# Kernel tuning notes

Measured on AMD Instinct MI355X. Metric: run time of the kernel, lower is better.

The kernel has to match this reference:

```python
import jax, jax.numpy as jnp
import numpy as np
from jax import lax

B, D, L = 32, 256, 4096
Q, H, T = D // 4, D // 2, 3 * D // 4


def setup_inputs() -> dict:
    key = jax.random.key(0)
    ks = iter(jax.random.split(key, 64))

    def nrm(shape, s=0.02):
        return jax.random.normal(next(ks), shape, jnp.float32) * s

    inp = {"x": jax.random.normal(next(ks), (B, D, L), jnp.float32)}

    def pw(name, o, c):  # pointwise conv: weight [O,C], bias [O]
        inp[name + "_w"] = nrm((o, c))
        inp[name + "_b"] = jnp.zeros((o,), jnp.float32)

    def dw(name, c, k):  # depthwise conv: weight [C,1,K], bias [C]
        inp[name + "_w"] = nrm((c, 1, k))
        inp[name + "_b"] = jnp.zeros((c,), jnp.float32)

    inp["ln1_w"] = jnp.ones((D,), jnp.float32); inp["ln1_b"] = jnp.zeros((D,), jnp.float32)
    pw("a1p", Q, Q); dw("a1d", Q, 7)
    pw("v1", Q, Q); pw("v11", Q, Q); pw("v12", Q, Q)
    dw("c31", Q, 3)
    inp["ln2_w"] = jnp.ones((H,), jnp.float32); inp["ln2_b"] = jnp.zeros((H,), jnp.float32)
    pw("a2p", H, H); dw("a2d", H, 9)
    pw("v2", H, H); pw("v21", H, H); pw("v22", Q, Q)
    pw("p2", Q, H)
    dw("c32", Q, 3)
    inp["ln3_w"] = jnp.ones((T,), jnp.float32); inp["ln3_b"] = jnp.zeros((T,), jnp.float32)
    pw("a3p", T, T); dw("a3d", T, 11)
    pw("v3", T, T); pw("v31", T, T); pw("v32", Q, Q)
    pw("p3", Q, T)
    dw("c33", Q, 3)
    return inp


def _ln_cf(x, w, b, eps=1e-6):
    # channels_first LayerNorm: normalize over channel dim (axis=1)
    u = jnp.mean(x, axis=1, keepdims=True)
    s = jnp.mean((x - u) ** 2, axis=1, keepdims=True)
    return w[:, None] * (x - u) / jnp.sqrt(s + eps) + b[:, None]


def _pw(x, w, b):
    # 1x1 conv1d: x [B,C,L], w [O,C] -> [B,O,L]
    return jnp.einsum('bcl,oc->bol', x, w) + b[:, None]


def _dw(x, w, b, pad):
    # depthwise conv1d: x [B,C,L], w [C,1,K]
    y = lax.conv_general_dilated(x, w, (1,), [(pad, pad)],
                                 dimension_numbers=('NCH', 'OIH', 'NCH'),
                                 feature_group_count=x.shape[1])
    return y + b[:, None]


def reference(x, ln1_w, ln1_b, a1p_w, a1p_b, a1d_w, a1d_b, v1_w, v1_b,
              v11_w, v11_b, v12_w, v12_b, c31_w, c31_b,
              ln2_w, ln2_b, a2p_w, a2p_b, a2d_w, a2d_b, v2_w, v2_b,
              v21_w, v21_b, v22_w, v22_b, p2_w, p2_b, c32_w, c32_b,
              ln3_w, ln3_b, a3p_w, a3p_b, a3d_w, a3d_b, v3_w, v3_b,
              v31_w, v31_b, v32_w, v32_b, p3_w, p3_b, c33_w, c33_b):
    x = _ln_cf(x, ln1_w, ln1_b)
    xs = jnp.split(x, 4, axis=1)  # 4 chunks of Q channels

    # stage 1
    a = _dw(jax.nn.gelu(_pw(xs[0], a1p_w, a1p_b), approximate=False), a1d_w, a1d_b, 3)
    mul = _pw(a * _pw(xs[0], v1_w, v1_b), v11_w, v11_b)
    x1 = _dw(_pw(xs[1], v12_w, v12_b), c31_w, c31_b, 1) + a
    x1 = jnp.concatenate([x1, mul], axis=1)  # [B,H,L]

    # stage 2
    x1 = _ln_cf(x1, ln2_w, ln2_b)
    a = _dw(jax.nn.gelu(_pw(x1, a2p_w, a2p_b), approximate=False), a2d_w, a2d_b, 4)
    mul = _pw(a * _pw(x1, v2_w, v2_b), v21_w, v21_b)
    x2 = _dw(_pw(xs[2], v22_w, v22_b), c32_w, c32_b, 1) + _pw(a, p2_w, p2_b)
    x2 = jnp.concatenate([x2, mul], axis=1)  # [B,T,L]

    # stage 3
    x2 = _ln_cf(x2, ln3_w, ln3_b)
    a = _dw(jax.nn.gelu(_pw(x2, a3p_w, a3p_b), approximate=False), a3d_w, a3d_b, 5)
    mul = _pw(a * _pw(x2, v3_w, v3_b), v31_w, v31_b)
    x3 = _dw(_pw(xs[3], v32_w, v32_b), c33_w, c33_b, 1) + _pw(a, p3_w, p3_b)
    return jnp.concatenate([x3, mul], axis=1)  # [B,D,L]
```

## Files before the change

kernel.cpp:

```cpp
#include <hip/hip_runtime.h>
#include <cmath>


using u16 = unsigned short;
typedef short shrt8 __attribute__((ext_vector_type(8)));
typedef short shrt4 __attribute__((ext_vector_type(4)));
typedef float f32x4 __attribute__((ext_vector_type(4)));

#define DEVI __device__ __forceinline__

static constexpr int TL   = 64;
static constexpr int EXT  = 88;
static constexpr int RS   = 72;
static constexpr int SLOT = EXT * RS;
static constexpr int NW   = 8;
static constexpr int NTHR = 512;

DEVI u16 f2bf(float f) {
    unsigned u = __float_as_uint(f);
    u += 0x7FFFu + ((u >> 16) & 1u);
    return (u16)(u >> 16);
}
DEVI float bf2f(u16 h) { return __uint_as_float(((unsigned)h) << 16); }

DEVI float gelu_f(float x) {
    const float y  = x * 0.70710678118654752f;
    const float ay = fabsf(y);
    const float t  = __builtin_amdgcn_rcpf(fmaf(0.3275911f, ay, 1.0f));
    float p = 1.061405429f;
    p = fmaf(p, t, -1.453152027f);
    p = fmaf(p, t,  1.421413741f);
    p = fmaf(p, t, -0.284496736f);
    p = fmaf(p, t,  0.254829592f);
    float er = 1.0f - p * t * __expf(-ay * ay);
    er = copysignf(er, y);
    return 0.5f * x * (1.0f + er);
}

struct SL { int a, b, c; };
DEVI int slotOf(SL s, int ch) { return ch < 64 ? s.a : (ch < 128 ? s.b : s.c); }

template<int O, int C, int OSPLIT, bool GELU, bool TOG, bool INPL, bool LNF>
DEVI void pw_mfma(u16* sh, SL in, SL outA, SL outB, const u16* Wb,
                  const float* biasA, const float* biasB,
                  int elo, int ehi, int l0,
                  const float* uv = nullptr, const float* rsA = nullptr,
                  const float* mrsA = nullptr,
                  float* outg = nullptr, int bidx = 0, int ochan = 0) {
    constexpr int MR = O / 64;
    constexpr int KT = C / 32;
    constexpr int NT = 3;
    const int lane = threadIdx.x & 63;
    const int wv   = threadIdx.x >> 6;
    const int mw = wv >> 1, nw = wv & 1;
    const int col  = lane & 15;
    const int quad = lane >> 4;
    const int mrow = mw * (MR * 16) + col;
    const int kq   = quad * 8;
    const int crow = mw * (MR * 16) + quad * 4;

    f32x4 acc[MR][NT];
    #pragma unroll
    for (int mi = 0; mi < MR; ++mi) {
        f32x4 bv;
        if (LNF) { bv[0] = 0.f; bv[1] = 0.f; bv[2] = 0.f; bv[3] = 0.f; }
        else {
            const int ch = crow + mi * 16;
            const float* bp = (OSPLIT < O && ch >= OSPLIT) ? (biasB + (ch - OSPLIT))
                                                           : (biasA + ch);
            bv = *(const f32x4*)bp;
        }
        #pragma unroll
        for (int ni = 0; ni < NT; ++ni) acc[mi][ni] = bv;
    }
    bool act[NT]; int bpos[NT];
    #pragma unroll
    for (int ni = 0; ni < NT; ++ni) {
        const int nt = nw * NT + ni;
        act[ni] = (nt * 16 < ehi) && (nt * 16 + 16 > elo);
        int p = nt * 16 + col; if (p > EXT - 1) p = EXT - 1;
        bpos[ni] = p;
    }
    __builtin_amdgcn_s_setprio(1);
    #pragma unroll
    for (int kt = 0; kt < KT; ++kt) {
        shrt8 af[MR];
        #pragma unroll
        for (int mi = 0; mi < MR; ++mi)
            af[mi] = *(const shrt8*)(Wb + (size_t)(mrow + mi * 16) * C + kt * 32 + kq);
        const int k0 = kt * 32;
        const u16* bs = sh + slotOf(in, k0) * SLOT + ((k0 & 63) + kq);
        #pragma unroll
        for (int ni = 0; ni < NT; ++ni) {
            if (!act[ni]) continue;
            const shrt8 bf = *(const shrt8*)(bs + bpos[ni] * RS);
            #pragma unroll
            for (int mi = 0; mi < MR; ++mi)
                acc[mi][ni] = __builtin_amdgcn_mfma_f32_16x16x32_bf16(af[mi], bf, acc[mi][ni], 0, 0, 0);
        }
    }
    __builtin_amdgcn_s_setprio(0);
    if (INPL) __syncthreads();
    float rsv[NT], mrsv[NT];
    if (LNF) {
        #pragma unroll
        for (int ni = 0; ni < NT; ++ni) {
            rsv[ni]  = rsA[bpos[ni]];
            mrsv[ni] = mrsA[bpos[ni]];
        }
    }
    #pragma unroll
    for (int mi = 0; mi < MR; ++mi) {
        const int ch = crow + mi * 16;
        const bool isA = !(OSPLIT < O) || (ch < OSPLIT);
        f32x4 u4, v4;
        if (LNF) {
            u4 = *(const f32x4*)(uv + ch);
            v4 = *(const f32x4*)(uv + O + ch);
        }
        #pragma unroll
        for (int ni = 0; ni < NT; ++ni) {
            if (!act[ni]) continue;
            const int e = (nw * NT + ni) * 16 + col;
            if (e < elo || e >= ehi) continue;
            const int l = l0 + e;
            f32x4 v = acc[mi][ni];
            if (LNF) {
                #pragma unroll
                for (int i = 0; i < 4; ++i)
                    v[i] = fmaf(rsv[ni], v[i], fmaf(-mrsv[ni], v4[i], u4[i]));
            }
            if (GELU && isA) { v[0]=gelu_f(v[0]); v[1]=gelu_f(v[1]); v[2]=gelu_f(v[2]); v[3]=gelu_f(v[3]); }
            if (TOG) {
                float* og = outg + ((size_t)bidx * 256 + ochan + ch) * 4096 + l;
                og[0] = v[0]; og[4096] = v[1]; og[2*4096] = v[2]; og[3*4096] = v[3];
            } else {
                const int cl = isA ? ch : ch - OSPLIT;
                const SL  os = isA ? outA : outB;
                const bool gv = (unsigned)l < 4096u;
                shrt4 pk;
                pk[0] = gv ? (short)f2bf(v[0]) : (short)0;
                pk[1] = gv ? (short)f2bf(v[1]) : (short)0;
                pk[2] = gv ? (short)f2bf(v[2]) : (short)0;
                pk[3] = gv ? (short)f2bf(v[3]) : (short)0;
                *(shrt4*)(sh + slotOf(os, cl) * SLOT + e * RS + (cl & 63)) = pk;
            }
        }
    }
}

template<int C, int K, int PAD, int WIN, bool INPL>
DEVI void dw_mul(u16* sh, SL g, SL ao, SL v, const float* W, const float* bias,
                 int elo, int ehi) {
    const int lane = threadIdx.x & 63;
    const int wv   = threadIdx.x >> 6;
    const int nwin  = (ehi - elo + WIN - 1) / WIN;
    const int tasks = (C / 64) * nwin;
    const bool have = wv < tasks;
    float r[K + WIN - 1];
    float wk[K];
    float bo = 0.f;
    int c = 0, e0 = 0;
    if (have) {
        const int cb = wv / nwin, wi = wv - cb * nwin;
        c = cb * 64 + lane;
        #pragma unroll
        for (int k = 0; k < K; ++k) wk[k] = W[c * K + k];
        bo = bias[c];
        e0 = elo + wi * WIN;
        const u16* si = sh + slotOf(g, c) * SLOT + lane;
        #pragma unroll
        for (int m = 0; m < K + WIN - 1; ++m) {
            int e = e0 - PAD + m; if (e > EXT - 1) e = EXT - 1;
            r[m] = bf2f(si[e * RS]);
        }
    }
    if (INPL) __syncthreads();
    if (have) {
        u16* sa = sh + slotOf(ao, c) * SLOT + lane;
        u16* sv = sh + slotOf(v, c) * SLOT + lane;
        #pragma unroll
        for (int j = 0; j < WIN; ++j) {
            const int e = e0 + j;
            if (e >= ehi) break;
            float acc = bo;
            #pragma unroll
            for (int k = 0; k < K; ++k) acc = fmaf(wk[k], r[j + k], acc);
            sa[e * RS] = f2bf(acc);
            sv[e * RS] = f2bf(acc * bf2f(sv[e * RS]));
        }
    }
}

template<int C, int K, int PAD, int WIN, bool ADD>
DEVI void dw_ph(u16* sh, SL in, SL add, SL out, const float* W, const float* bias,
                int elo, int ehi, int l0) {
    const int lane = threadIdx.x & 63;
    const int wv   = threadIdx.x >> 6;
    const int nwin = (ehi - elo + WIN - 1) / WIN;
    const int tasks = (C / 64) * nwin;
    for (int t = wv; t < tasks; t += NW) {
        const int cb = t / nwin, wi = t - cb * nwin;
        const int c = cb * 64 + lane;
        float wk[K];
        #pragma unroll
        for (int k = 0; k < K; ++k) wk[k] = W[c * K + k];
        const float bo = bias[c];
        const int e0 = elo + wi * WIN;
        const u16* si = sh + slotOf(in, c) * SLOT + lane;
        const u16* sa = ADD ? (sh + slotOf(add, c) * SLOT + lane) : nullptr;
        u16* so = sh + slotOf(out, c) * SLOT + lane;
        float r[K + WIN - 1];
        #pragma unroll
        for (int m = 0; m < K + WIN - 1; ++m) {
            int e = e0 - PAD + m; if (e > EXT - 1) e = EXT - 1;
            r[m] = bf2f(si[e * RS]);
        }
        #pragma unroll
        for (int j = 0; j < WIN; ++j) {
            const int e = e0 + j;
            if (e >= ehi) break;
            float acc = bo;
            #pragma unroll
            for (int k = 0; k < K; ++k) acc = fmaf(wk[k], r[j + k], acc);
            if (ADD) acc += bf2f(sa[e * RS]);
            const bool gv = (unsigned)(l0 + e) < 4096u;
            so[e * RS] = gv ? f2bf(acc) : (u16)0;
        }
    }
}

template<int C>
DEVI void ln_stats(u16* sh, SL s, int elo, int ehi, float* scr,
                   float* muRS, float* rs) {
    constexpr int P = C / 64;
    const int tid = threadIdx.x;
    const int nP = ehi - elo;
    if (tid < nP * P) {
        const int e = elo + tid / P;
        const int part = tid - (tid / P) * P;
        const u16* row = sh + slotOf(s, part * 64) * SLOT + e * RS;
        float sm = 0.f, sq = 0.f;
        #pragma unroll
        for (int j = 0; j < 8; ++j) {
            shrt8 v = *(const shrt8*)(row + j * 8);
            #pragma unroll
            for (int i = 0; i < 8; ++i) { float f = bf2f((u16)v[i]); sm += f; sq += f * f; }
        }
        scr[tid * 2] = sm; scr[tid * 2 + 1] = sq;
    }
    __syncthreads();
    if (tid < nP) {
        float sm = 0.f, sq = 0.f;
        for (int p = 0; p < P; ++p) { sm += scr[(tid * P + p) * 2]; sq += scr[(tid * P + p) * 2 + 1]; }
        const float mu = sm * (1.0f / C);
        const float va = sq * (1.0f / C) - mu * mu;
        const float r = rsqrtf(va + 1e-6f);
        rs[elo + tid] = r; muRS[elo + tid] = mu * r;
    }
}

DEVI void norm_load(u16* sh, int slot, const float* xg, int b, int cbase,
                    const float* lnw, const float* lnb,
                    const float* mean, const float* rstd,
                    int elo, int ehi, int l0) {
    const int lane = threadIdx.x & 63;
    const int wv   = threadIdx.x >> 6;
    #pragma unroll
    for (int j = 0; j < 8; ++j) {
        const int o = wv + NW * j;
        const float* p = xg + ((size_t)b * 256 + cbase + o) * 4096;
        const float wo = lnw[cbase + o], bo = lnb[cbase + o];
        u16* r = sh + slot * SLOT + o;
        #pragma unroll
        for (int part = 0; part < 2; ++part) {
            const int e = elo + lane + part * 64;
            if (e < ehi) {
                const int l = l0 + e;
                const bool gv = (unsigned)l < 4096u;
                float v = gv ? p[l] : 0.f;
                v = (v - mean[e]) * rstd[e] * wo + bo;
                r[e * RS] = gv ? f2bf(v) : (u16)0;
            }
        }
    }
}

DEVI void dw3_glob(u16* sh, int inSlot, int addSlot, const float* W, const float* B,
                   float* outg, int b, int l0) {
    const int tid = threadIdx.x;
    #pragma unroll
    for (int k = 0; k < 8; ++k) {
        const int idx = tid + k * NTHR;
        const int c   = idx >> 6;
        const int e   = 12 + (idx & 63);
        const u16* si = sh + inSlot * SLOT + c;
        float acc = B[c];
        acc = fmaf(W[c * 3 + 0], bf2f(si[(e - 1) * RS]), acc);
        acc = fmaf(W[c * 3 + 1], bf2f(si[e * RS]), acc);
        acc = fmaf(W[c * 3 + 2], bf2f(si[(e + 1) * RS]), acc);
        acc += bf2f(sh[addSlot * SLOT + e * RS + c]);
        outg[((size_t)b * 256 + c) * 4096 + (l0 + e)] = acc;
    }
}


enum {
    I_X = 0, I_LN1W, I_LN1B, I_A1PW, I_A1PB, I_A1DW, I_A1DB, I_V1W, I_V1B,
    I_V11W, I_V11B, I_V12W, I_V12B, I_C31W, I_C31B,
    I_LN2W, I_LN2B, I_A2PW, I_A2PB, I_A2DW, I_A2DB, I_V2W, I_V2B,
    I_V21W, I_V21B, I_V22W, I_V22B, I_P2W, I_P2B, I_C32W, I_C32B,
    I_LN3W, I_LN3B, I_A3PW, I_A3PB, I_A3DW, I_A3DB, I_V3W, I_V3B,
    I_V31W, I_V31B, I_V32W, I_V32B, I_P3W, I_P3B, I_C33W, I_C33B
};
enum { W_A1P = 0, W_V1, W_V11, W_V12, W_A2P, W_V2, W_V21, W_V22, W_P2,
       W_A3P, W_V3, W_V31, W_V32, W_P3, W_N };

struct KArgs {
    const float* p[47]; const u16* w[W_N]; const float* stats;
    const float* uvA2; const float* uvV2; const float* uvA3; const float* uvV3;
    float* out;
};
struct CvtArgs {
    const float* src[W_N]; const float* scl[W_N]; u16* dst;
    int off[W_N + 1]; int cdim[W_N];
};
struct UVArgs {
    const float *w2a, *w2b, *b2a, *b2b, *ln2b;
    const float *w3a, *w3b, *b3a, *b3b, *ln3b;
    const u16 *f2a, *f2b, *f3a, *f3b;
    float *uvA2, *uvV2, *uvA3, *uvV3;
};

__global__ __launch_bounds__(256) void cvt_kernel(CvtArgs a) {
    const int i = blockIdx.x * 256 + threadIdx.x;
    if (i >= a.off[W_N]) return;
    int s = 0;
    while (i >= a.off[s + 1]) ++s;
    const int j = i - a.off[s];
    float v = a.src[s][j];
    if (a.scl[s]) {
        const int cd = a.cdim[s];
        v *= a.scl[s][j - (j / cd) * cd];
    }
    a.dst[i] = f2bf(v);
}

__global__ __launch_bounds__(64) void uv_kernel(UVArgs a) {
    const int blk  = blockIdx.x;
    const int lane = threadIdx.x;
    int o, C; const float *row, *lnb; const u16 *fr; float bias;
    float *uo, *vo;
    if (blk < 128) {
        o = blk; C = 128; row = a.w2a + (size_t)o * 128; lnb = a.ln2b;
        fr = a.f2a + (size_t)o * 128; bias = a.b2a[o];
        uo = a.uvA2 + o; vo = a.uvA2 + 128 + o;
    } else if (blk < 256) {
        o = blk - 128; C = 128; row = a.w2b + (size_t)o * 128; lnb = a.ln2b;
        fr = a.f2b + (size_t)o * 128; bias = a.b2b[o];
        uo = a.uvV2 + o; vo = a.uvV2 + 128 + o;
    } else if (blk < 448) {
        o = blk - 256; C = 192; row = a.w3a + (size_t)o * 192; lnb = a.ln3b;
        fr = a.f3a + (size_t)o * 192; bias = a.b3a[o];
        uo = a.uvA3 + o; vo = a.uvA3 + 192 + o;
    } else {
        o = blk - 448; C = 192; row = a.w3b + (size_t)o * 192; lnb = a.ln3b;
        fr = a.f3b + (size_t)o * 192; bias = a.b3b[o];
        uo = a.uvV3 + o; vo = a.uvV3 + 192 + o;
    }
    float u = 0.f, v = 0.f;
    for (int c = lane; c < C; c += 64) { u += row[c] * lnb[c]; v += bf2f(fr[c]); }
    #pragma unroll
    for (int off = 32; off; off >>= 1) {
        u += __shfl_down(u, off);
        v += __shfl_down(v, off);
    }
    if (lane == 0) { *uo = bias + u; *vo = v; }
}

__global__ __launch_bounds__(256) void ln1pre_kernel(const float* x, float* stats) {
    __shared__ float red[512];
    const int b    = blockIdx.x >> 6;
    const int lb   = blockIdx.x & 63;
    const int lidx = threadIdx.x & 63;
    const int cg   = threadIdx.x >> 6;
    const int l    = lb * 64 + lidx;
    const float* p = x + ((size_t)b * 256 + cg * 64) * 4096 + l;
    float sm = 0.f, sq = 0.f;
    #pragma unroll 8
    for (int c = 0; c < 64; ++c) {
        const float v = p[(size_t)c * 4096];
        sm += v; sq += v * v;
    }
    red[threadIdx.x * 2]     = sm;
    red[threadIdx.x * 2 + 1] = sq;
    __syncthreads();
    if (threadIdx.x < 64) {
        float s = 0.f, q = 0.f;
        #pragma unroll
        for (int g = 0; g < 4; ++g) {
            s += red[(g * 64 + lidx) * 2];
            q += red[(g * 64 + lidx) * 2 + 1];
        }
        const float mu = s * (1.0f / 256.0f);
        const float va = q * (1.0f / 256.0f) - mu * mu;
        float2 o; o.x = mu; o.y = rsqrtf(va + 1e-6f);
        *(float2*)(stats + 2 * ((size_t)b * 4096 + l)) = o;
    }
}

__global__ __launch_bounds__(NTHR, 4) void convmod_kernel(KArgs a) {
    __shared__ u16 pool[6 * SLOT];
    __shared__ float meanA[EXT], rstdA[EXT], muRSB[EXT], rsB[EXT];
    __shared__ float scr[448];

    const int b    = blockIdx.x >> 6;
    const int tile = blockIdx.x & 63;
    const int l0   = tile * TL - 12;
    const float* xg = a.p[I_X];
    u16* sh = pool;

    if (threadIdx.x < EXT) {
        const int l = l0 + (int)threadIdx.x;
        float mu = 0.f, rs = 1.f;
        if ((unsigned)l < 4096u) {
            const float2 st = *(const float2*)(a.stats + 2 * ((size_t)b * 4096 + l));
            mu = st.x; rs = st.y;
        }
        meanA[threadIdx.x] = mu; rstdA[threadIdx.x] = rs;
    }
    __syncthreads();
    norm_load(sh, 0, xg, b,  0, a.p[I_LN1W], a.p[I_LN1B], meanA, rstdA, 0, EXT, l0);
    norm_load(sh, 1, xg, b, 64, a.p[I_LN1W], a.p[I_LN1B], meanA, rstdA, 0, EXT, l0);
    __syncthreads();
    pw_mfma<128, 64, 64, true, false, false, false>(sh, SL{0,-1,-1}, SL{2,-1,-1}, SL{3,-1,-1},
        a.w[W_A1P], a.p[I_A1PB], a.p[I_V1B], 0, 88, l0);
    pw_mfma<64, 64, 64, false, false, false, false>(sh, SL{1,-1,-1}, SL{4,-1,-1}, SL{4,-1,-1},
        a.w[W_V12], a.p[I_V12B], a.p[I_V12B], 2, 86, l0);
    __syncthreads();
    dw_mul<64, 7, 3, 16, false>(sh, SL{2,-1,-1}, SL{5,-1,-1}, SL{3,-1,-1}, a.p[I_A1DW], a.p[I_A1DB], 3, 85);
    __syncthreads();
    pw_mfma<64, 64, 64, false, false, false, false>(sh, SL{3,-1,-1}, SL{2,-1,-1}, SL{2,-1,-1},
        a.w[W_V11], a.p[I_V11B], a.p[I_V11B], 3, 85, l0);
    dw_ph<64, 3, 1, 11, true>(sh, SL{4,-1,-1}, SL{5,-1,-1}, SL{1,-1,-1}, a.p[I_C31W], a.p[I_C31B], 3, 85, l0);
    __syncthreads();
    ln_stats<128>(sh, SL{1,2,-1}, 3, 85, scr, muRSB, rsB);
    __syncthreads();
    norm_load(sh, 0, xg, b, 128, a.p[I_LN1W], a.p[I_LN1B], meanA, rstdA, 6, 82, l0);
    pw_mfma<128, 128, 128, true, false, false, true>(sh, SL{1,2,-1}, SL{3,4,-1}, SL{3,4,-1},
        a.w[W_A2P], nullptr, nullptr, 3, 85, l0, a.uvA2, rsB, muRSB);
    pw_mfma<128, 128, 128, false, false, true, true>(sh, SL{1,2,-1}, SL{1,2,-1}, SL{1,2,-1},
        a.w[W_V2], nullptr, nullptr, 7, 81, l0, a.uvV2, rsB, muRSB);
    __syncthreads();
    pw_mfma<64, 64, 64, false, false, false, false>(sh, SL{0,-1,-1}, SL{5,-1,-1}, SL{5,-1,-1},
        a.w[W_V22], a.p[I_V22B], a.p[I_V22B], 6, 82, l0);
    dw_mul<128, 9, 4, 19, true>(sh, SL{3,4,-1}, SL{3,4,-1}, SL{1,2,-1}, a.p[I_A2DW], a.p[I_A2DB], 7, 81);
    __syncthreads();
    pw_mfma<64, 128, 64, false, false, false, false>(sh, SL{3,4,-1}, SL{0,-1,-1}, SL{0,-1,-1},
        a.w[W_P2], a.p[I_P2B], a.p[I_P2B], 7, 81, l0);
    pw_mfma<128, 128, 128, false, false, true, false>(sh, SL{1,2,-1}, SL{1,2,-1}, SL{1,2,-1},
        a.w[W_V21], a.p[I_V21B], a.p[I_V21B], 7, 81, l0);
    __syncthreads();
    dw_ph<64, 3, 1, 10, true>(sh, SL{5,-1,-1}, SL{0,-1,-1}, SL{3,-1,-1}, a.p[I_C32W], a.p[I_C32B], 7, 81, l0);
    __syncthreads();
    ln_stats<192>(sh, SL{3,1,2}, 7, 81, scr, muRSB, rsB);
    __syncthreads();
    pw_mfma<192, 192, 192, true, false, false, true>(sh, SL{3,1,2}, SL{4,5,0}, SL{4,5,0},
        a.w[W_A3P], nullptr, nullptr, 7, 81, l0, a.uvA3, rsB, muRSB);
    pw_mfma<192, 192, 192, false, false, true, true>(sh, SL{3,1,2}, SL{3,1,2}, SL{3,1,2},
        a.w[W_V3], nullptr, nullptr, 12, 76, l0, a.uvV3, rsB, muRSB);
    __syncthreads();
    dw_mul<192, 11, 5, 32, true>(sh, SL{4,5,0}, SL{4,5,0}, SL{3,1,2}, a.p[I_A3DW], a.p[I_A3DB], 12, 76);
    __syncthreads();
    pw_mfma<192, 192, 192, false, true, false, false>(sh, SL{3,1,2}, SL{-1,-1,-1}, SL{-1,-1,-1},
        a.w[W_V31], a.p[I_V31B], a.p[I_V31B], 12, 76, l0,
        nullptr, nullptr, nullptr, a.out, b, 64);
    pw_mfma<64, 192, 64, false, false, true, false>(sh, SL{4,5,0}, SL{4,-1,-1}, SL{4,-1,-1},
        a.w[W_P3], a.p[I_P3B], a.p[I_P3B], 12, 76, l0);
    norm_load(sh, 5, xg, b, 192, a.p[I_LN1W], a.p[I_LN1B], meanA, rstdA, 11, 77, l0);
    __syncthreads();
    pw_mfma<64, 64, 64, false, false, false, false>(sh, SL{5,-1,-1}, SL{0,-1,-1}, SL{0,-1,-1},
        a.w[W_V32], a.p[I_V32B], a.p[I_V32B], 11, 77, l0);
    __syncthreads();
    dw3_glob(sh, 0, 4, a.p[I_C33W], a.p[I_C33B], a.out, b, l0);
}

extern "C" void kernel_launch(void* const* d_in, const int* in_sizes, int n_in,
                              void* d_out, int out_size, void* d_ws, size_t ws_size,
                              hipStream_t stream) {
    (void)in_sizes; (void)n_in; (void)out_size; (void)ws_size;
    static const int widx[W_N] = { I_A1PW, I_V1W, I_V11W, I_V12W, I_A2PW, I_V2W,
                                   I_V21W, I_V22W, I_P2W, I_A3PW, I_V3W, I_V31W,
                                   I_V32W, I_P3W };
    static const int wsz[W_N]  = { 4096, 4096, 4096, 4096, 16384, 16384, 16384,
                                   4096, 8192, 36864, 36864, 36864, 4096, 12288 };
    static const int wcd[W_N]  = { 64, 64, 64, 64, 128, 128, 128, 64, 128,
                                   192, 192, 192, 64, 192 };
    CvtArgs ca; KArgs ka;
    int off = 0;
    for (int i = 0; i < W_N; ++i) {
        ca.src[i]  = (const float*)d_in[widx[i]];
        ca.scl[i]  = nullptr;
        ca.cdim[i] = wcd[i];
        ca.off[i]  = off;
        off += wsz[i];
    }
    ca.scl[W_A2P] = (const float*)d_in[I_LN2W];
    ca.scl[W_V2]  = (const float*)d_in[I_LN2W];
    ca.scl[W_A3P] = (const float*)d_in[I_LN3W];
    ca.scl[W_V3]  = (const float*)d_in[I_LN3W];
    ca.off[W_N] = off;
    ca.dst = (u16*)d_ws;
    for (int i = 0; i < 47; ++i) ka.p[i] = (const float*)d_in[i];
    for (int i = 0; i < W_N; ++i) ka.w[i] = (const u16*)d_ws + ca.off[i];
    const size_t stats_off = ((size_t)off * sizeof(u16) + 255) & ~(size_t)255;
    float* stats = (float*)((char*)d_ws + stats_off);
    float* uvA2  = stats + (size_t)32 * 4096 * 2;
    float* uvV2  = uvA2 + 256;
    float* uvA3  = uvV2 + 256;
    float* uvV3  = uvA3 + 384;
    ka.stats = stats;
    ka.uvA2 = uvA2; ka.uvV2 = uvV2; ka.uvA3 = uvA3; ka.uvV3 = uvV3;
    ka.out = (float*)d_out;

    UVArgs ua;
    ua.w2a = (const float*)d_in[I_A2PW]; ua.w2b = (const float*)d_in[I_V2W];
    ua.b2a = (const float*)d_in[I_A2PB]; ua.b2b = (const float*)d_in[I_V2B];
    ua.ln2b = (const float*)d_in[I_LN2B];
    ua.w3a = (const float*)d_in[I_A3PW]; ua.w3b = (const float*)d_in[I_V3W];
    ua.b3a = (const float*)d_in[I_A3PB]; ua.b3b = (const float*)d_in[I_V3B];
    ua.ln3b = (const float*)d_in[I_LN3B];
    ua.f2a = (const u16*)d_ws + ca.off[W_A2P];
    ua.f2b = (const u16*)d_ws + ca.off[W_V2];
    ua.f3a = (const u16*)d_ws + ca.off[W_A3P];
    ua.f3b = (const u16*)d_ws + ca.off[W_V3];
    ua.uvA2 = uvA2; ua.uvV2 = uvV2; ua.uvA3 = uvA3; ua.uvV3 = uvV3;

    cvt_kernel<<<dim3((off + 255) / 256), dim3(256), 0, stream>>>(ca);
    uv_kernel<<<dim3(640), dim3(64), 0, stream>>>(ua);
    ln1pre_kernel<<<dim3(32 * 64), dim3(256), 0, stream>>>((const float*)d_in[I_X], stats);
    convmod_kernel<<<dim3(32 * 64), dim3(NTHR), 0, stream>>>(ka);
}
```

Before: 694.7 us.

## Prefetch x chunks into registers ahead of compute and drop MFMA setprio

```diff
diff --git a/kernel.cpp b/kernel.cpp
--- a/kernel.cpp
+++ b/kernel.cpp
@@ -81,7 +81,6 @@
         int p = nt * 16 + col; if (p > EXT - 1) p = EXT - 1;
         bpos[ni] = p;
     }
-    __builtin_amdgcn_s_setprio(1);
     #pragma unroll
     for (int kt = 0; kt < KT; ++kt) {
         shrt8 af[MR];
@@ -99,7 +98,6 @@
                 acc[mi][ni] = __builtin_amdgcn_mfma_f32_16x16x32_bf16(af[mi], bf, acc[mi][ni], 0, 0, 0);
         }
     }
-    __builtin_amdgcn_s_setprio(0);
     if (INPL) __syncthreads();
     float rsv[NT], mrsv[NT];
     if (LNF) {
@@ -286,6 +284,46 @@
     }
 }
 
+DEVI void nl_issue(float* xr, const float* xg, int b, int cbase,
+                   int elo, int ehi, int l0) {
+    const int lane = threadIdx.x & 63;
+    const int wv   = threadIdx.x >> 6;
+    #pragma unroll
+    for (int j = 0; j < 8; ++j) {
+        const int o = wv + NW * j;
+        const float* p = xg + ((size_t)b * 256 + cbase + o) * 4096;
+        #pragma unroll
+        for (int part = 0; part < 2; ++part) {
+            const int e = elo + lane + part * 64;
+            const int l = l0 + e;
+            xr[j * 2 + part] = (e < ehi && (unsigned)l < 4096u) ? p[l] : 0.f;
+        }
+    }
+}
+DEVI void nl_write(u16* sh, int slot, const float* xr, int cbase,
+                   const float* lnw, const float* lnb,
+                   const float* mean, const float* rstd,
+                   int elo, int ehi, int l0) {
+    const int lane = threadIdx.x & 63;
+    const int wv   = threadIdx.x >> 6;
+    #pragma unroll
+    for (int j = 0; j < 8; ++j) {
+        const int o = wv + NW * j;
+        const float wo = lnw[cbase + o], bo = lnb[cbase + o];
+        u16* r = sh + slot * SLOT + o;
+        #pragma unroll
+        for (int part = 0; part < 2; ++part) {
+            const int e = elo + lane + part * 64;
+            if (e < ehi) {
+                const int l = l0 + e;
+                const bool gv = (unsigned)l < 4096u;
+                float v = (xr[j * 2 + part] - mean[e]) * rstd[e] * wo + bo;
+                r[e * RS] = gv ? f2bf(v) : (u16)0;
+            }
+        }
+    }
+}
+
 DEVI void dw3_glob(u16* sh, int inSlot, int addSlot, const float* W, const float* B,
                    float* outg, int b, int l0) {
     const int tid = threadIdx.x;
@@ -438,7 +476,12 @@
     pw_mfma<64, 64, 64, false, false, false, false>(sh, SL{1,-1,-1}, SL{4,-1,-1}, SL{4,-1,-1},
         a.w[W_V12], a.p[I_V12B], a.p[I_V12B], 2, 86, l0);
     __syncthreads();
-    dw_mul<64, 7, 3, 16, false>(sh, SL{2,-1,-1}, SL{5,-1,-1}, SL{3,-1,-1}, a.p[I_A1DW], a.p[I_A1DB], 3, 85);
+    {
+        float xr[16];
+        nl_issue(xr, xg, b, 128, 6, 82, l0);
+        dw_mul<64, 7, 3, 16, false>(sh, SL{2,-1,-1}, SL{5,-1,-1}, SL{3,-1,-1}, a.p[I_A1DW], a.p[I_A1DB], 3, 85);
+        nl_write(sh, 0, xr, 128, a.p[I_LN1W], a.p[I_LN1B], meanA, rstdA, 6, 82, l0);
+    }
     __syncthreads();
     pw_mfma<64, 64, 64, false, false, false, false>(sh, SL{3,-1,-1}, SL{2,-1,-1}, SL{2,-1,-1},
         a.w[W_V11], a.p[I_V11B], a.p[I_V11B], 3, 85, l0);
@@ -446,7 +489,6 @@
     __syncthreads();
     ln_stats<128>(sh, SL{1,2,-1}, 3, 85, scr, muRSB, rsB);
     __syncthreads();
-    norm_load(sh, 0, xg, b, 128, a.p[I_LN1W], a.p[I_LN1B], meanA, rstdA, 6, 82, l0);
     pw_mfma<128, 128, 128, true, false, false, true>(sh, SL{1,2,-1}, SL{3,4,-1}, SL{3,4,-1},
         a.w[W_A2P], nullptr, nullptr, 3, 85, l0, a.uvA2, rsB, muRSB);
     pw_mfma<128, 128, 128, false, false, true, true>(sh, SL{1,2,-1}, SL{1,2,-1}, SL{1,2,-1},
@@ -472,12 +514,16 @@
     __syncthreads();
     dw_mul<192, 11, 5, 32, true>(sh, SL{4,5,0}, SL{4,5,0}, SL{3,1,2}, a.p[I_A3DW], a.p[I_A3DB], 12, 76);
     __syncthreads();
-    pw_mfma<192, 192, 192, false, true, false, false>(sh, SL{3,1,2}, SL{-1,-1,-1}, SL{-1,-1,-1},
-        a.w[W_V31], a.p[I_V31B], a.p[I_V31B], 12, 76, l0,
-        nullptr, nullptr, nullptr, a.out, b, 64);
-    pw_mfma<64, 192, 64, false, false, true, false>(sh, SL{4,5,0}, SL{4,-1,-1}, SL{4,-1,-1},
-        a.w[W_P3], a.p[I_P3B], a.p[I_P3B], 12, 76, l0);
-    norm_load(sh, 5, xg, b, 192, a.p[I_LN1W], a.p[I_LN1B], meanA, rstdA, 11, 77, l0);
+    {
+        float xr[16];
+        nl_issue(xr, xg, b, 192, 11, 77, l0);
+        pw_mfma<192, 192, 192, false, true, false, false>(sh, SL{3,1,2}, SL{-1,-1,-1}, SL{-1,-1,-1},
+            a.w[W_V31], a.p[I_V31B], a.p[I_V31B], 12, 76, l0,
+            nullptr, nullptr, nullptr, a.out, b, 64);
+        pw_mfma<64, 192, 64, false, false, true, false>(sh, SL{4,5,0}, SL{4,-1,-1}, SL{4,-1,-1},
+            a.w[W_P3], a.p[I_P3B], a.p[I_P3B], 12, 76, l0);
+        nl_write(sh, 5, xr, 192, a.p[I_LN1W], a.p[I_LN1B], meanA, rstdA, 11, 77, l0);
+    }
     __syncthreads();
     pw_mfma<64, 64, 64, false, false, false, false>(sh, SL{5,-1,-1}, SL{0,-1,-1}, SL{0,-1,-1},
         a.w[W_V32], a.p[I_V32B], a.p[I_V32B], 11, 77, l0);
```

Result: faster. 663.5 us (-4.5%).
